# Optimization experiments

Hardware: AMD Instinct MI355X
Metric: run time of the kernel (lower is better)

Reference implementation:

```python
import jax, jax.numpy as jnp
import numpy as np

N = 4096          # batch size / number of points
D_DATA = 1024     # data feature dim
D_LATENT = 64     # latent dim
REG_LAMBDA = 0.5


def _pdist(x):
    """Pairwise Euclidean distance matrix [N, N] via the gram trick.

    Equivalent to norm(x[None, :, :] - x[:, None, :], axis=-1) but avoids the
    N x N x D intermediate. Safe sqrt so the (zero) diagonal has zero gradient.
    """
    sq = jnp.sum(x * x, axis=-1)                      # [N]
    g = x @ x.T                                       # [N, N] gram
    d2 = jnp.maximum(sq[:, None] + sq[None, :] - 2.0 * g, 0.0)
    pos = d2 > 0
    d = jnp.sqrt(jnp.where(pos, d2, 1.0))
    return jnp.where(pos, d, 0.0)


def _mst_edges(dist):
    """Edges (i, j) of the minimum spanning tree of the complete graph with
    edge weights dist[i, j] (0d persistent homology death edges).
    Prim's algorithm, vectorized per step via lax.scan. Returns [N-1, 2] int32.
    """
    n = dist.shape[0]
    in_tree = jnp.zeros(n, dtype=bool).at[0].set(True)
    min_dist = dist[0]                                # best distance to tree
    min_src = jnp.zeros(n, dtype=jnp.int32)           # tree node achieving it

    def step(carry, _):
        in_tree, min_dist, min_src = carry
        masked = jnp.where(in_tree, jnp.inf, min_dist)
        j = jnp.argmin(masked).astype(jnp.int32)
        edge = jnp.stack([min_src[j], j])
        in_tree = in_tree.at[j].set(True)
        dj = dist[j]
        upd = dj < min_dist
        min_dist = jnp.where(upd, dj, min_dist)
        min_src = jnp.where(upd, j, min_src)
        return (in_tree, min_dist, min_src), edge

    _, edges = jax.lax.scan(step, (in_tree, min_dist, min_src), None, length=n - 1)
    return edges  # [N-1, 2]


def _gather(dist, edges):
    return dist[edges[:, 0], edges[:, 1]]  # [N-1]


def setup_inputs() -> dict:
    key = jax.random.key(0)
    k1, k2, k3 = jax.random.split(key, 3)
    return {
        "y_true": jax.random.normal(k1, (N, D_DATA), dtype=jnp.float32),
        "latent": jax.random.normal(k2, (N, D_LATENT), dtype=jnp.float32),
        "y_pred": jax.random.normal(k3, (N, D_DATA), dtype=jnp.float32),
        "latent_norm": jnp.array(1.0, dtype=jnp.float32),
    }


def reference(y_true, latent, y_pred, latent_norm):
    # keras MSE: mean over last axis -> per-sample vector [N]
    ae_loss = jnp.mean((y_true - y_pred) ** 2, axis=-1)

    data_distances = _pdist(y_true)
    data_distances = data_distances / jnp.max(data_distances)
    latent_distances = _pdist(latent) / latent_norm

    e_data = _mst_edges(jax.lax.stop_gradient(data_distances))
    data_loss = jnp.mean((_gather(data_distances, e_data)
                          - _gather(latent_distances, e_data)) ** 2)

    e_lat = _mst_edges(jax.lax.stop_gradient(latent_distances))
    latent_loss = jnp.mean((_gather(data_distances, e_lat)
                            - _gather(latent_distances, e_lat)) ** 2)

    topo_loss = data_loss + latent_loss
    return ae_loss + REG_LAMBDA * topo_loss  # [N] (scalar topo broadcast)
```

## Files before the change

### kernel.cpp

```cpp
#include <hip/hip_runtime.h>
#include <math.h>

#define N_PTS 4096
#define DD 1024
#define DL 64
#define NEDGE (N_PTS - 1)
#define B_ROUNDS 12
#define NT 32

typedef __attribute__((ext_vector_type(8))) short short8;
typedef __attribute__((ext_vector_type(4))) float floatx4;
typedef __attribute__((ext_vector_type(4))) unsigned short ushortx4;

__device__ __forceinline__ unsigned short f2bf(float f) {
  unsigned u = __float_as_uint(f);
  u = u + 0x7FFFu + ((u >> 16) & 1u);
  return (unsigned short)(u >> 16);
}

__global__ __launch_bounds__(256) void ae_sq_kernel(const float* __restrict__ yt,
                                                    const float* __restrict__ yp,
                                                    float* __restrict__ out,
                                                    float* __restrict__ sqD,
                                                    unsigned short* __restrict__ Xb) {
  int row = blockIdx.x, tid = threadIdx.x;
  const float4* a = (const float4*)(yt + (size_t)row * DD);
  const float4* b = (const float4*)(yp + (size_t)row * DD);
  float4 va = a[tid], vb = b[tid];
  ushortx4 o = {f2bf(va.x), f2bf(va.y), f2bf(va.z), f2bf(va.w)};
  *(ushortx4*)(Xb + (size_t)row * DD + tid * 4) = o;
  float e0 = va.x - vb.x, e1 = va.y - vb.y, e2 = va.z - vb.z, e3 = va.w - vb.w;
  float se = e0 * e0 + e1 * e1 + e2 * e2 + e3 * e3;
  float ss = va.x * va.x + va.y * va.y + va.z * va.z + va.w * va.w;
  for (int off = 32; off > 0; off >>= 1) {
    se += __shfl_down(se, off);
    ss += __shfl_down(ss, off);
  }
  __shared__ float sse[4], sss[4];
  int lane = tid & 63, w = tid >> 6;
  if (lane == 0) { sse[w] = se; sss[w] = ss; }
  __syncthreads();
  if (tid == 0) {
    out[row] = (sse[0] + sse[1] + sse[2] + sse[3]) * (1.0f / DD);
    sqD[row] = sss[0] + sss[1] + sss[2] + sss[3];
  }
}

__global__ __launch_bounds__(256) void sql_kernel(const float* __restrict__ lat,
                                                  float* __restrict__ sqL,
                                                  unsigned short* __restrict__ Lb) {
  int row = blockIdx.x * 4 + (threadIdx.x >> 6);
  int lane = threadIdx.x & 63;
  float v = lat[(size_t)row * DL + lane];
  Lb[(size_t)row * DL + lane] = f2bf(v);
  float s = v * v;
  for (int off = 32; off > 0; off >>= 1) s += __shfl_down(s, off);
  if (lane == 0) sqL[row] = s;
}

__global__ __launch_bounds__(1024) void norm_kernel(const float* __restrict__ sqD,
                                                    const float* __restrict__ sqL,
                                                    unsigned int* __restrict__ normbits) {
  const float* s = blockIdx.x ? sqL : sqD;
  int tid = threadIdx.x;
  float m = fmaxf(fmaxf(s[tid], s[tid + 1024]), fmaxf(s[tid + 2048], s[tid + 3072]));
  for (int off = 32; off > 0; off >>= 1) m = fmaxf(m, __shfl_down(m, off));
  __shared__ float sm[16];
  int lane = tid & 63, w = tid >> 6;
  if (lane == 0) sm[w] = m;
  __syncthreads();
  if (tid == 0) {
    float mm = sm[0];
    for (int k = 1; k < 16; ++k) mm = fmaxf(mm, sm[k]);
    normbits[blockIdx.x] = __float_as_uint(mm);
  }
}

__global__ __launch_bounds__(256) void dist_mfma(const unsigned short* __restrict__ Xb,
                                                 const unsigned short* __restrict__ Lb,
                                                 const float* __restrict__ sqD,
                                                 const float* __restrict__ sqL,
                                                 unsigned short* __restrict__ dD,
                                                 unsigned short* __restrict__ dL,
                                                 const unsigned int* __restrict__ normbits,
                                                 unsigned int* __restrict__ maxbits) {
  int inst = blockIdx.y;
  const unsigned short* X = inst ? Lb : Xb;
  const float* sq = inst ? sqL : sqD;
  unsigned short* dist = inst ? dL : dD;
  int K = inst ? DL : DD;
  float scale = 65535.0f / (2.0f * sqrtf(__uint_as_float(normbits[inst])) + 1e-12f);

  int bi = 0, rem = blockIdx.x, span = NT;
  while (rem >= span) { rem -= span; ++bi; --span; }
  int bj = bi + rem;
  int row0 = bi * 128, col0 = bj * 128;

  __shared__ short As[128 * 40];
  __shared__ short Bs[128 * 40];
  int tid = threadIdx.x;
  int wave = tid >> 6, lane = tid & 63;
  int m = lane & 15, q = lane >> 4;
  int rw = (wave >> 1) * 64, cw = (wave & 1) * 64;

  floatx4 acc[4][4];
#pragma unroll
  for (int mi = 0; mi < 4; ++mi)
#pragma unroll
    for (int ni = 0; ni < 4; ++ni) acc[mi][ni] = {0.f, 0.f, 0.f, 0.f};

  int s0 = tid, s1 = tid + 256;
  int r0 = s0 >> 2, p0 = s0 & 3, r1 = s1 >> 2, p1 = s1 & 3;

  for (int k0 = 0; k0 < K; k0 += 32) {
    short8 a0 = *(const short8*)(X + (size_t)(row0 + r0) * K + k0 + p0 * 8);
    short8 a1 = *(const short8*)(X + (size_t)(row0 + r1) * K + k0 + p1 * 8);
    short8 b0 = *(const short8*)(X + (size_t)(col0 + r0) * K + k0 + p0 * 8);
    short8 b1 = *(const short8*)(X + (size_t)(col0 + r1) * K + k0 + p1 * 8);
    __syncthreads();
    *(short8*)&As[r0 * 40 + p0 * 8] = a0;
    *(short8*)&As[r1 * 40 + p1 * 8] = a1;
    *(short8*)&Bs[r0 * 40 + p0 * 8] = b0;
    *(short8*)&Bs[r1 * 40 + p1 * 8] = b1;
    __syncthreads();
    short8 aF[4], bF[4];
#pragma unroll
    for (int mi = 0; mi < 4; ++mi)
      aF[mi] = *(const short8*)&As[(rw + mi * 16 + m) * 40 + q * 8];
#pragma unroll
    for (int ni = 0; ni < 4; ++ni)
      bF[ni] = *(const short8*)&Bs[(cw + ni * 16 + m) * 40 + q * 8];
#pragma unroll
    for (int mi = 0; mi < 4; ++mi)
#pragma unroll
      for (int ni = 0; ni < 4; ++ni)
        acc[mi][ni] = __builtin_amdgcn_mfma_f32_16x16x32_bf16(aF[mi], bF[ni],
                                                              acc[mi][ni], 0, 0, 0);
  }

  float bmax = 0.f;
#pragma unroll
  for (int mi = 0; mi < 4; ++mi) {
    int i0 = row0 + rw + mi * 16 + q * 4;
    float s_i[4] = {sq[i0], sq[i0 + 1], sq[i0 + 2], sq[i0 + 3]};
#pragma unroll
    for (int ni = 0; ni < 4; ++ni) {
      int j = col0 + cw + ni * 16 + m;
      float sj = sq[j];
      ushortx4 tvec;
#pragma unroll
      for (int r = 0; r < 4; ++r) {
        float d2 = s_i[r] + sj - 2.f * acc[mi][ni][r];
        float d = d2 > 0.f ? sqrtf(d2) : 0.f;
        bmax = fmaxf(bmax, d);
        unsigned short u = (unsigned short)fminf(d * scale, 65535.0f);
        dist[(size_t)(i0 + r) * N_PTS + j] = u;
        tvec[r] = u;
      }
      *(ushortx4*)&dist[(size_t)j * N_PTS + i0] = tvec;
    }
  }
  if (inst == 0) {
    for (int off = 32; off > 0; off >>= 1) bmax = fmaxf(bmax, __shfl_down(bmax, off));
    __shared__ float bm[4];
    if (lane == 0) bm[wave] = bmax;
    __syncthreads();
    if (tid == 0)
      atomicMax(maxbits, __float_as_uint(fmaxf(fmaxf(bm[0], bm[1]), fmaxf(bm[2], bm[3]))));
  }
}

__global__ __launch_bounds__(256) void boruvka_init(unsigned short* __restrict__ comp,
                                                    unsigned long long* __restrict__ bestKey,
                                                    int* __restrict__ numRoots,
                                                    int* __restrict__ edgeCnt) {
  int i = blockIdx.x * 256 + threadIdx.x;
  if (i < N_PTS) {
    comp[i] = (unsigned short)i;
    comp[N_PTS + i] = (unsigned short)i;
    bestKey[i] = ~0ULL;
    bestKey[N_PTS + i] = ~0ULL;
  }
  if (i == 0) {
    numRoots[0] = N_PTS; numRoots[1] = N_PTS;
    edgeCnt[0] = 0; edgeCnt[1] = 0;
  }
}

__global__ __launch_bounds__(256) void boruvka_scan0(const unsigned short* __restrict__ dD,
                                                     const unsigned short* __restrict__ dL,
                                                     unsigned int* __restrict__ segKey,
                                                     unsigned long long* __restrict__ bestKey) {
  int inst = blockIdx.y;
  const unsigned short* dist = inst ? dL : dD;
  unsigned int* segK = segKey + (size_t)inst * N_PTS * 64;
  unsigned long long* bkI = bestKey + (size_t)inst * N_PTS;
  int tid = threadIdx.x, wave = tid >> 6, lane = tid & 63;
  int row = blockIdx.x * 4 + wave;
  const uint4* rowp = (const uint4*)(dist + (size_t)row * N_PTS);
  unsigned mk = 0xFFFFFFFFu, fk = 0xFFFFFFFFu;
  int colbase = lane * 64;
#pragma unroll
  for (int t = 0; t < 8; ++t) {
    uint4 v = rowp[lane * 8 + t];
    unsigned e[8] = {v.x & 0xFFFFu, v.x >> 16, v.y & 0xFFFFu, v.y >> 16,
                     v.z & 0xFFFFu, v.z >> 16, v.w & 0xFFFFu, v.w >> 16};
#pragma unroll
    for (int u = 0; u < 8; ++u) {
      int col = colbase + t * 8 + u;
      unsigned key = (e[u] << 12) | (unsigned)col;
      mk = min(mk, key);
      if (col != row) fk = min(fk, key);
    }
  }
  segK[(size_t)row * 64 + lane] = mk;
#pragma unroll
  for (int off = 32; off > 0; off >>= 1) fk = min(fk, __shfl_xor(fk, off));
  if (lane == 0) {
    unsigned dd16 = fk >> 12;
    int j = (int)(fk & 0xFFFu);
    int lo = row < j ? row : j, hi = row < j ? j : row;
    bkI[row] = ((unsigned long long)dd16 << 24) |
               ((unsigned long long)lo << 12) | (unsigned long long)hi;
  }
}

__global__ __launch_bounds__(256) void boruvka_scan(const unsigned short* __restrict__ dD,
                                                    const unsigned short* __restrict__ dL,
                                                    const unsigned int* __restrict__ segKey,
                                                    const unsigned short* __restrict__ comp,
                                                    unsigned long long* __restrict__ bestKey,
                                                    const int* __restrict__ numRoots) {
  int inst = blockIdx.y;
  if (numRoots[inst] <= 1) return;
  const unsigned short* dist = inst ? dL : dD;
  const unsigned int* segK = segKey + (size_t)inst * N_PTS * 64;
  const unsigned short* compI = comp + (size_t)inst * N_PTS;
  unsigned long long* bkI = bestKey + (size_t)inst * N_PTS;
  int tid = threadIdx.x, wave = tid >> 6, lane = tid & 63;

  int row = blockIdx.x * 4 + wave;
  unsigned myc = compI[row];
  unsigned skey = segK[(size_t)row * 64 + lane];
#pragma unroll
  for (int k = 2; k <= 64; k <<= 1)
#pragma unroll
    for (int j = k >> 1; j > 0; j >>= 1) {
      unsigned p = __shfl_xor(skey, j);
      unsigned mn = min(skey, p), mx = max(skey, p);
      skey = (((lane & k) == 0) == ((lane & j) == 0)) ? mn : mx;
    }
  unsigned best = 0xFFFFFFFFu;
  const unsigned short* rowp = dist + (size_t)row * N_PTS;
  int i = 0;
  while (i < 64) {
    unsigned k0 = __shfl(skey, i);
    if (k0 >= best) break;
    unsigned k1 = (i < 63) ? __shfl(skey, i + 1) : 0xFFFFFFFFu;
    int b0 = (int)(k0 & 0xFC0u);
    unsigned d0v = rowp[b0 + lane];
    unsigned c0v = compI[b0 + lane];
    unsigned cand = (c0v != myc) ? ((d0v << 12) | (unsigned)(b0 + lane)) : 0xFFFFFFFFu;
    if (k1 < best) {
      int b1 = (int)(k1 & 0xFC0u);
      unsigned d1v = rowp[b1 + lane];
      unsigned c1v = compI[b1 + lane];
      unsigned c2 = (c1v != myc) ? ((d1v << 12) | (unsigned)(b1 + lane)) : 0xFFFFFFFFu;
      cand = min(cand, c2);
    }
#pragma unroll
    for (int off = 32; off > 0; off >>= 1) cand = min(cand, __shfl_xor(cand, off));
    best = min(best, cand);
    i += 2;
  }
  if (lane == 0 && best != 0xFFFFFFFFu) {
    unsigned dd16 = best >> 12;
    int j = (int)(best & 0xFFFu);
    int lo = row < j ? row : j, hi = row < j ? j : row;
    unsigned long long key40 = ((unsigned long long)dd16 << 24) |
                               ((unsigned long long)lo << 12) | (unsigned long long)hi;
    if (key40 < bkI[myc]) atomicMin(&bkI[myc], key40);
  }
}

__global__ __launch_bounds__(1024) void boruvka_merge(unsigned short* __restrict__ comp,
                                                      unsigned long long* __restrict__ bestKey,
                                                      int* __restrict__ numRoots,
                                                      int2* __restrict__ edges,
                                                      int* __restrict__ edgeCnt) {
  int inst = blockIdx.x;
  if (numRoots[inst] <= 1) return;
  unsigned short* compI = comp + (size_t)inst * N_PTS;
  unsigned long long* bkI = bestKey + (size_t)inst * N_PTS;
  edges += (size_t)inst * NEDGE;

  __shared__ unsigned short comp_s[N_PTS];
  __shared__ unsigned short parent_s[N_PTS];
  __shared__ unsigned long long key_s[N_PTS];
  __shared__ int scn[1024];
  __shared__ int rootCnt;
  int tid = threadIdx.x;
  if (tid == 0) rootCnt = 0;
  for (int i = tid; i < N_PTS / 4; i += 1024)
    ((uint2*)comp_s)[i] = ((const uint2*)compI)[i];
  for (int i = tid; i < N_PTS / 2; i += 1024)
    ((uint4*)key_s)[i] = ((const uint4*)bkI)[i];
  __syncthreads();

  int cnt = 0;
  int2 ebuf[4];
#pragma unroll
  for (int k = 0; k < 4; ++k) {
    int c = tid + k * 1024;
    unsigned short p = (unsigned short)c;
    if (comp_s[c] == c) {
      unsigned long long key = key_s[c];
      bkI[c] = ~0ULL;
      if (key != ~0ULL) {
        int lo = (int)((key >> 12) & 0xFFF), hi = (int)(key & 0xFFF);
        int c2 = (comp_s[lo] == c) ? comp_s[hi] : comp_s[lo];
        bool mutual = (key_s[c2] == key);
        bool add;
        if (mutual) {
          if (c < c2) add = true;
          else { p = (unsigned short)c2; add = false; }
        } else { p = (unsigned short)c2; add = true; }
        if (add) ebuf[cnt++] = make_int2(lo, hi);
      }
    }
    parent_s[c] = p;
  }
  scn[tid] = cnt;
  __syncthreads();
  for (int s = 1; s < 1024; s <<= 1) {
    int v = (tid >= s) ? scn[tid - s] : 0;
    __syncthreads();
    scn[tid] += v;
    __syncthreads();
  }
  int base = edgeCnt[inst] + scn[tid] - cnt;
  for (int k = 0; k < cnt; ++k)
    if (base + k < NEDGE) edges[base + k] = ebuf[k];
  if (tid == 1023) edgeCnt[inst] += scn[1023];
  for (int it = 0; it < 12; ++it) {
    __syncthreads();
#pragma unroll
    for (int k = 0; k < 4; ++k) {
      int c = tid + k * 1024;
      parent_s[c] = parent_s[parent_s[c]];
    }
  }
  __syncthreads();
  int local = 0;
#pragma unroll
  for (int k = 0; k < 4; ++k) {
    int c = tid + k * 1024;
    compI[c] = parent_s[comp_s[c]];
    if (comp_s[c] == c && parent_s[c] == c) local++;
  }
  atomicAdd(&rootCnt, local);
  __syncthreads();
  if (tid == 0) numRoots[inst] = rootCnt;
}

__global__ __launch_bounds__(256) void loss_kernel(const unsigned short* __restrict__ dD,
                                                   const unsigned short* __restrict__ dL,
                                                   const int2* __restrict__ edges_all,
                                                   const unsigned int* __restrict__ maxbits,
                                                   const unsigned int* __restrict__ normbits,
                                                   const float* __restrict__ latent_norm,
                                                   float* __restrict__ sums) {
  int tid = threadIdx.x;
  int e = blockIdx.x * 256 + tid;
  float facD = (2.0f * sqrtf(__uint_as_float(normbits[0])) + 1e-12f) * (1.0f / 65535.0f) /
               __uint_as_float(*maxbits);
  float facL = (2.0f * sqrtf(__uint_as_float(normbits[1])) + 1e-12f) * (1.0f / 65535.0f) /
               latent_norm[0];
  float v0 = 0.f, v1 = 0.f;
  if (e < 2 * NEDGE) {
    int2 ed = edges_all[e];
    int i = ed.x & (N_PTS - 1), j = ed.y & (N_PTS - 1);
    float dd = (float)dD[(size_t)i * N_PTS + j] * facD;
    float ld = (float)dL[(size_t)i * N_PTS + j] * facL;
    float df = dd - ld;
    if (e < NEDGE) v0 = df * df; else v1 = df * df;
  }
  for (int off = 32; off > 0; off >>= 1) {
    v0 += __shfl_down(v0, off);
    v1 += __shfl_down(v1, off);
  }
  __shared__ float s0[4], s1[4];
  int lane = tid & 63, w = tid >> 6;
  if (lane == 0) { s0[w] = v0; s1[w] = v1; }
  __syncthreads();
  if (tid == 0) {
    float t0 = s0[0] + s0[1] + s0[2] + s0[3];
    float t1 = s1[0] + s1[1] + s1[2] + s1[3];
    if (t0 != 0.f) atomicAdd(&sums[0], t0);
    if (t1 != 0.f) atomicAdd(&sums[1], t1);
  }
}

__global__ __launch_bounds__(256) void finalize_kernel(float* __restrict__ out,
                                                       const float* __restrict__ sums) {
  int i = blockIdx.x * blockDim.x + threadIdx.x;
  float topo = (sums[0] + sums[1]) * (1.0f / NEDGE);
  out[i] += 0.5f * topo;
}

extern "C" void kernel_launch(void* const* d_in, const int* in_sizes, int n_in,
                              void* d_out, int out_size, void* d_ws, size_t ws_size,
                              hipStream_t stream) {
  const float* y_true = (const float*)d_in[0];
  const float* latent = (const float*)d_in[1];
  const float* y_pred = (const float*)d_in[2];
  const float* latent_norm = (const float*)d_in[3];
  float* out = (float*)d_out;
  char* ws = (char*)d_ws;

  const size_t MAT16 = (size_t)N_PTS * N_PTS * 2;
  size_t off = 0;
  unsigned short* dD = (unsigned short*)(ws + off); off += MAT16;
  unsigned short* dL = (unsigned short*)(ws + off); off += MAT16;
  unsigned short* Xb = (unsigned short*)(ws + off); off += (size_t)N_PTS * DD * 2;
  unsigned short* Lb = (unsigned short*)(ws + off); off += (size_t)N_PTS * DL * 2;
  float* sqD = (float*)(ws + off); off += (size_t)N_PTS * 4;
  float* sqL = (float*)(ws + off); off += (size_t)N_PTS * 4;
  int2* edges = (int2*)(ws + off); off += (size_t)2 * NEDGE * 8 + 16;
  unsigned long long* bestKey = (unsigned long long*)(ws + off); off += (size_t)2 * N_PTS * 8;
  unsigned short* comp = (unsigned short*)(ws + off); off += (size_t)2 * N_PTS * 2;
  unsigned int* segKey = (unsigned int*)(ws + off); off += (size_t)2 * N_PTS * 64 * 4;
  int* numRoots = (int*)(ws + off); off += 256;
  int* edgeCnt = numRoots + 2;
  unsigned int* maxbits = (unsigned int*)(edgeCnt + 2);
  float* sums = (float*)(maxbits + 1);
  unsigned int* normbits = (unsigned int*)(sums + 2);

  hipMemsetAsync(numRoots, 0, 256, stream);

  ae_sq_kernel<<<N_PTS, 256, 0, stream>>>(y_true, y_pred, out, sqD, Xb);
  sql_kernel<<<N_PTS / 4, 256, 0, stream>>>(latent, sqL, Lb);
  norm_kernel<<<2, 1024, 0, stream>>>(sqD, sqL, normbits);
  boruvka_init<<<N_PTS / 256, 256, 0, stream>>>(comp, bestKey, numRoots, edgeCnt);

  int tri = NT * (NT + 1) / 2;
  dist_mfma<<<dim3(tri, 2), 256, 0, stream>>>(Xb, Lb, sqD, sqL, dD, dL, normbits, maxbits);

  boruvka_scan0<<<dim3(N_PTS / 4, 2), 256, 0, stream>>>(dD, dL, segKey, bestKey);
  boruvka_merge<<<2, 1024, 0, stream>>>(comp, bestKey, numRoots, edges, edgeCnt);
  for (int r = 1; r < B_ROUNDS; ++r) {
    boruvka_scan<<<dim3(N_PTS / 4, 2), 256, 0, stream>>>(dD, dL, segKey, comp, bestKey,
                                                         numRoots);
    boruvka_merge<<<2, 1024, 0, stream>>>(comp, bestKey, numRoots, edges, edgeCnt);
  }

  loss_kernel<<<32, 256, 0, stream>>>(dD, dL, edges, maxbits, normbits, latent_norm, sums);
  finalize_kernel<<<N_PTS / 256, 256, 0, stream>>>(out, sums);
}
```

Measured before the change: 285.6 us.

## Stage transposed distance tile in LDS, fuse norm into init, speed merge scan

The distance kernel now writes the mirrored (transposed) half of each tile through a per-wave shared-memory staging buffer, so it can be stored with coalesced 16-byte row writes instead of scattered 8-byte column writes. The norm-max reduction is folded into boruvka_init, which removes one kernel launch. In the merge kernel, the 1024-wide shared-memory Hillis-Steele scan is replaced by a wave-shuffle scan plus a serial combine of 16 wave totals. Pointer jumping now exits early once no parent changes, and the root count is reduced with shuffles before the atomic. Costs: the MFMA kernel uses more shared memory (about 36KB per block), which may lower occupancy, and it adds an extra barrier.

```diff
diff --git a/kernel.cpp b/kernel.cpp
--- a/kernel.cpp
+++ b/kernel.cpp
@@ -58,21 +58,37 @@
   if (lane == 0) sqL[row] = s;
 }
 
-__global__ __launch_bounds__(1024) void norm_kernel(const float* __restrict__ sqD,
+__global__ __launch_bounds__(256) void boruvka_init(unsigned short* __restrict__ comp,
+                                                    unsigned long long* __restrict__ bestKey,
+                                                    int* __restrict__ numRoots,
+                                                    int* __restrict__ edgeCnt,
+                                                    const float* __restrict__ sqD,
                                                     const float* __restrict__ sqL,
                                                     unsigned int* __restrict__ normbits) {
-  const float* s = blockIdx.x ? sqL : sqD;
-  int tid = threadIdx.x;
-  float m = fmaxf(fmaxf(s[tid], s[tid + 1024]), fmaxf(s[tid + 2048], s[tid + 3072]));
-  for (int off = 32; off > 0; off >>= 1) m = fmaxf(m, __shfl_down(m, off));
-  __shared__ float sm[16];
-  int lane = tid & 63, w = tid >> 6;
-  if (lane == 0) sm[w] = m;
-  __syncthreads();
-  if (tid == 0) {
-    float mm = sm[0];
-    for (int k = 1; k < 16; ++k) mm = fmaxf(mm, sm[k]);
-    normbits[blockIdx.x] = __float_as_uint(mm);
+  int i = blockIdx.x * 256 + threadIdx.x;
+  if (i < N_PTS) {
+    comp[i] = (unsigned short)i;
+    comp[N_PTS + i] = (unsigned short)i;
+    bestKey[i] = ~0ULL;
+    bestKey[N_PTS + i] = ~0ULL;
+  }
+  if (i == 0) {
+    numRoots[0] = N_PTS; numRoots[1] = N_PTS;
+    edgeCnt[0] = 0; edgeCnt[1] = 0;
+  }
+  if (blockIdx.x < 2) {
+    const float* s = blockIdx.x ? sqL : sqD;
+    int tid = threadIdx.x;
+    float m = 0.f;
+#pragma unroll
+    for (int k = 0; k < 16; ++k) m = fmaxf(m, s[tid + k * 256]);
+    for (int off = 32; off > 0; off >>= 1) m = fmaxf(m, __shfl_down(m, off));
+    __shared__ float sm[4];
+    int lane = tid & 63, w = tid >> 6;
+    if (lane == 0) sm[w] = m;
+    __syncthreads();
+    if (tid == 0)
+      normbits[blockIdx.x] = __float_as_uint(fmaxf(fmaxf(sm[0], sm[1]), fmaxf(sm[2], sm[3])));
   }
 }
 
@@ -96,8 +112,9 @@
   int bj = bi + rem;
   int row0 = bi * 128, col0 = bj * 128;
 
-  __shared__ short As[128 * 40];
-  __shared__ short Bs[128 * 40];
+  __shared__ short smem[18432];
+  short* As = smem;
+  short* Bs = smem + 5120;
   int tid = threadIdx.x;
   int wave = tid >> 6, lane = tid & 63;
   int m = lane & 15, q = lane >> 4;
@@ -137,7 +154,9 @@
         acc[mi][ni] = __builtin_amdgcn_mfma_f32_16x16x32_bf16(aF[mi], bF[ni],
                                                               acc[mi][ni], 0, 0, 0);
   }
-
+  __syncthreads();
+
+  unsigned short* tw = (unsigned short*)smem + wave * 4608;
   float bmax = 0.f;
 #pragma unroll
   for (int mi = 0; mi < 4; ++mi) {
@@ -147,19 +166,25 @@
     for (int ni = 0; ni < 4; ++ni) {
       int j = col0 + cw + ni * 16 + m;
       float sj = sq[j];
-      ushortx4 tvec;
 #pragma unroll
       for (int r = 0; r < 4; ++r) {
         float d2 = s_i[r] + sj - 2.f * acc[mi][ni][r];
         float d = d2 > 0.f ? sqrtf(d2) : 0.f;
         bmax = fmaxf(bmax, d);
-        unsigned short u = (unsigned short)fminf(d * scale, 65535.0f);
-        dist[(size_t)(i0 + r) * N_PTS + j] = u;
-        tvec[r] = u;
+        unsigned u = (unsigned)fminf(d * scale, 65535.0f);
+        dist[(size_t)(i0 + r) * N_PTS + j] = (unsigned short)u;
+        tw[(ni * 16 + m) * 72 + mi * 16 + q * 4 + r] = (unsigned short)u;
       }
-      *(ushortx4*)&dist[(size_t)j * N_PTS + i0] = tvec;
-    }
-  }
+    }
+  }
+  {
+    int jrow = col0 + cw + lane;
+    uint4* dst = (uint4*)(dist + (size_t)jrow * N_PTS + row0 + rw);
+    const uint4* src = (const uint4*)(tw + lane * 72);
+#pragma unroll
+    for (int t = 0; t < 8; ++t) dst[t] = src[t];
+  }
+
   if (inst == 0) {
     for (int off = 32; off > 0; off >>= 1) bmax = fmaxf(bmax, __shfl_down(bmax, off));
     __shared__ float bm[4];
@@ -167,23 +192,6 @@
     __syncthreads();
     if (tid == 0)
       atomicMax(maxbits, __float_as_uint(fmaxf(fmaxf(bm[0], bm[1]), fmaxf(bm[2], bm[3]))));
-  }
-}
-
-__global__ __launch_bounds__(256) void boruvka_init(unsigned short* __restrict__ comp,
-                                                    unsigned long long* __restrict__ bestKey,
-                                                    int* __restrict__ numRoots,
-                                                    int* __restrict__ edgeCnt) {
-  int i = blockIdx.x * 256 + threadIdx.x;
-  if (i < N_PTS) {
-    comp[i] = (unsigned short)i;
-    comp[N_PTS + i] = (unsigned short)i;
-    bestKey[i] = ~0ULL;
-    bestKey[N_PTS + i] = ~0ULL;
-  }
-  if (i == 0) {
-    numRoots[0] = N_PTS; numRoots[1] = N_PTS;
-    edgeCnt[0] = 0; edgeCnt[1] = 0;
   }
 }
 
@@ -297,12 +305,12 @@
   __shared__ unsigned short comp_s[N_PTS];
   __shared__ unsigned short parent_s[N_PTS];
   __shared__ unsigned long long key_s[N_PTS];
-  __shared__ int scn[1024];
-  __shared__ int rootCnt;
-  int tid = threadIdx.x;
+  __shared__ int wtot[16], wbase[16];
+  __shared__ int rootCnt, changed;
+  int tid = threadIdx.x, lane = tid & 63, w = tid >> 6;
   if (tid == 0) rootCnt = 0;
-  for (int i = tid; i < N_PTS / 4; i += 1024)
-    ((uint2*)comp_s)[i] = ((const uint2*)compI)[i];
+  for (int i = tid; i < N_PTS / 8; i += 1024)
+    ((uint4*)comp_s)[i] = ((const uint4*)compI)[i];
   for (int i = tid; i < N_PTS / 2; i += 1024)
     ((uint4*)key_s)[i] = ((const uint4*)bkI)[i];
   __syncthreads();
@@ -330,35 +338,48 @@
     }
     parent_s[c] = p;
   }
-  scn[tid] = cnt;
-  __syncthreads();
-  for (int s = 1; s < 1024; s <<= 1) {
-    int v = (tid >= s) ? scn[tid - s] : 0;
-    __syncthreads();
-    scn[tid] += v;
-    __syncthreads();
-  }
-  int base = edgeCnt[inst] + scn[tid] - cnt;
+  int ws = cnt;
+#pragma unroll
+  for (int off = 1; off < 64; off <<= 1) {
+    int v = __shfl_up(ws, off);
+    if (lane >= off) ws += v;
+  }
+  if (lane == 63) wtot[w] = ws;
+  __syncthreads();
+  if (tid == 0) {
+    int acc = edgeCnt[inst];
+    for (int k = 0; k < 16; ++k) { wbase[k] = acc; acc += wtot[k]; }
+    edgeCnt[inst] = acc;
+  }
+  __syncthreads();
+  int base = wbase[w] + ws - cnt;
   for (int k = 0; k < cnt; ++k)
     if (base + k < NEDGE) edges[base + k] = ebuf[k];
-  if (tid == 1023) edgeCnt[inst] += scn[1023];
   for (int it = 0; it < 12; ++it) {
-    __syncthreads();
+    if (tid == 0) changed = 0;
+    __syncthreads();
+    int any = 0;
 #pragma unroll
     for (int k = 0; k < 4; ++k) {
       int c = tid + k * 1024;
-      parent_s[c] = parent_s[parent_s[c]];
-    }
-  }
-  __syncthreads();
+      unsigned short p = parent_s[c];
+      unsigned short pp = parent_s[p];
+      if (pp != p) { parent_s[c] = pp; any = 1; }
+    }
+    if (any) changed = 1;
+    __syncthreads();
+    if (!changed) break;
+  }
   int local = 0;
 #pragma unroll
   for (int k = 0; k < 4; ++k) {
     int c = tid + k * 1024;
-    compI[c] = parent_s[comp_s[c]];
-    if (comp_s[c] == c && parent_s[c] == c) local++;
-  }
-  atomicAdd(&rootCnt, local);
+    unsigned short old = comp_s[c];
+    if (old == (unsigned short)c && parent_s[c] == (unsigned short)c) local++;
+    compI[c] = parent_s[old];
+  }
+  for (int off = 32; off > 0; off >>= 1) local += __shfl_down(local, off);
+  if (lane == 0) atomicAdd(&rootCnt, local);
   __syncthreads();
   if (tid == 0) numRoots[inst] = rootCnt;
 }
@@ -440,8 +461,8 @@
 
   ae_sq_kernel<<<N_PTS, 256, 0, stream>>>(y_true, y_pred, out, sqD, Xb);
   sql_kernel<<<N_PTS / 4, 256, 0, stream>>>(latent, sqL, Lb);
-  norm_kernel<<<2, 1024, 0, stream>>>(sqD, sqL, normbits);
-  boruvka_init<<<N_PTS / 256, 256, 0, stream>>>(comp, bestKey, numRoots, edgeCnt);
+  boruvka_init<<<N_PTS / 256, 256, 0, stream>>>(comp, bestKey, numRoots, edgeCnt,
+                                                sqD, sqL, normbits);
 
   int tri = NT * (NT + 1) / 2;
   dist_mfma<<<dim3(tri, 2), 256, 0, stream>>>(Xb, Lb, sqD, sqL, dD, dL, normbits, maxbits);
```

After: 281.7 us. About the same (-1.4%).
